# Optimization experiments

Hardware: AMD Instinct MI355X
Metric: run time of the kernel (lower is better)

The kernel has to match this reference:

```python
import jax, jax.numpy as jnp
import numpy as np

T, N, D, V = 512, 256, 1024, 128000  # total tokens, sampled tokens, d_model, vocab


def setup_inputs() -> dict:
    key = jax.random.key(0)
    k1, k2, k3, k4, k5 = jax.random.split(key, 5)
    hidden_states = jax.random.normal(k1, (T, D), dtype=jnp.float32)
    embedding = jax.random.normal(k2, (V, D), dtype=jnp.float32) * 0.02
    # temperatures in [0.5, 1.5): realistic, avoids divide blow-up (0.0 maps to 1.0 in source)
    temperatures = 0.5 + jax.random.uniform(k3, (N,), dtype=jnp.float32)
    # top_p in [0.5, 1.0)
    top_ps = 0.5 + 0.5 * jax.random.uniform(k4, (N,), dtype=jnp.float32)
    last_token_indices = jnp.sort(jax.random.randint(k5, (N,), 0, T))
    return {
        "hidden_states": hidden_states,
        "embedding": embedding,
        "temperatures": temperatures,
        "top_ps": top_ps,
        "last_token_indices": last_token_indices,
    }


def reference(hidden_states, embedding, temperatures, top_ps, last_token_indices):
    # gather last-token hidden states, project to vocab logits
    h = hidden_states[last_token_indices]              # [N, D]
    logits = jnp.einsum("nd,vd->nv", h, embedding)     # [N, V]
    # temperature softmax
    probs = jax.nn.softmax(logits / temperatures[:, None], axis=-1)
    # top-p: descending sort, cumsum, mask tail, renormalize, un-sort
    order = jnp.argsort(-probs, axis=-1)               # descending order indices
    probs_sort = jnp.take_along_axis(probs, order, axis=-1)
    cum = jnp.cumsum(probs_sort, axis=-1)
    mask = (cum - probs_sort) > top_ps[:, None]
    probs_sort = jnp.where(mask, 0.0, probs_sort)
    probs_sort = probs_sort / jnp.sum(probs_sort, axis=-1, keepdims=True)
    inv = jnp.argsort(order, axis=-1)                  # inverse permutation
    probs_f = jnp.take_along_axis(probs_sort, inv, axis=-1)
    # multinomial sampling (one token per row), fixed key for determinism
    tokens = jax.random.categorical(jax.random.key(42), jnp.log(probs_f + 1e-20), axis=-1)
    return probs_f, tokens
```

## Files before the change

### kernel.cpp

```cpp
#include <hip/hip_runtime.h>
#include <stdint.h>

#define N_TOK 256
#define D_MODEL 1024
#define VOCAB 128000
#define NV_ELEMS (256LL * 128000LL)
#define LIST_CAP 24576
#define GLIST_CAP 16384

typedef unsigned long long u64;
typedef uint32_t u32;
typedef __attribute__((ext_vector_type(8))) short bfrag;
typedef __attribute__((ext_vector_type(4))) float facc;

__device__ __forceinline__ uint32_t bf16_rne_bits(float x) {
    uint32_t u = __float_as_uint(x);
    return (u + 0x7fffu + ((u >> 16) & 1u)) >> 16;
}

__device__ __forceinline__ uint32_t rotl32(uint32_t x, int d) {
    return (x << d) | (x >> (32 - d));
}

__device__ __forceinline__ u32 mono32(u32 b) {
    return (b & 0x80000000u) ? ~b : (b | 0x80000000u);
}
__device__ __forceinline__ float unmono32(u32 k) {
    u32 b = (k & 0x80000000u) ? (k & 0x7FFFFFFFu) : ~k;
    return __uint_as_float(b);
}

__device__ __forceinline__ u64 fixmass(float rv) {
    return (u64)(rv * 1073741824.0f);
}

__device__ __forceinline__ uint2 tf_0_42(uint32_t c0, uint32_t c1) {
    const uint32_t ks0 = 0u, ks1 = 42u, ks2 = 0x1BD11BDAu ^ 42u;
    uint32_t x0 = c0 + ks0, x1 = c1 + ks1;
#define R4(a,b,c,d) \
    x0 += x1; x1 = rotl32(x1,a); x1 ^= x0; \
    x0 += x1; x1 = rotl32(x1,b); x1 ^= x0; \
    x0 += x1; x1 = rotl32(x1,c); x1 ^= x0; \
    x0 += x1; x1 = rotl32(x1,d); x1 ^= x0;
    R4(13,15,26,6)   x0 += ks1; x1 += ks2 + 1u;
    R4(17,29,16,24)  x0 += ks2; x1 += ks0 + 2u;
    R4(13,15,26,6)   x0 += ks0; x1 += ks1 + 3u;
    R4(17,29,16,24)  x0 += ks1; x1 += ks2 + 4u;
    R4(13,15,26,6)   x0 += ks2; x1 += ks0 + 5u;
#undef R4
    return make_uint2(x0, x1);
}

__device__ __forceinline__ uint32_t jax_bits(uint32_t j) {
    uint2 r = tf_0_42(0u, j);
    return r.x ^ r.y;
}

__device__ __forceinline__ float jax_gumbel(uint32_t bits) {
    const float TINY = 1.17549435e-38f;
    float u = __uint_as_float((bits >> 9) | 0x3f800000u) - 1.0f;
    u = u + TINY;
    u = fmaxf(TINY, u);
    return -__logf(-__logf(u));
}

__device__ __forceinline__ float rv_of(float l, float rinv) {
    return __expf(l * rinv);
}

__device__ __forceinline__ void async_copy16(const void* g, void* lbase, int lane) {
#if defined(__has_builtin) && __has_builtin(__builtin_amdgcn_global_load_lds)
    __builtin_amdgcn_global_load_lds((const uint32_t*)g, (uint32_t*)lbase, 16, 0, 0);
#else
    *(bfrag*)((char*)lbase + lane * 16) = *(const bfrag*)g;
#endif
}

__device__ __forceinline__ void scan_desc_u64(const u64* h, int nb, u64 carry, u64 P,
                                              int* outCb, u64* outSa) {
    int lane = (int)threadIdx.x & 63;
    int chunk = nb >> 6;
    int top = nb - 1 - lane * chunk;
    u64 ls = 0ull;
    for (int j = 0; j < chunk; ++j) ls += h[top - j];
    u64 incl = ls;
    for (int o = 1; o < 64; o <<= 1) {
        u64 v = __shfl_up(incl, o, 64);
        if (lane >= o) incl += v;
    }
    u64 s0 = carry + incl - ls;
    unsigned long long mask = __ballot(s0 + ls > P);
    if (mask == 0ull) {
        if (lane == 0) { *outCb = 0; *outSa = carry; }
    } else {
        int cstar = (int)__builtin_ctzll(mask);
        if (lane == cstar) {
            u64 sa = s0; int cb = 0;
            for (int j = 0; j < chunk; ++j) {
                int b = top - j;
                if (sa + h[b] > P) { cb = b; break; }
                sa += h[b];
            }
            *outCb = cb; *outSa = sa;
        }
    }
}

__global__ __launch_bounds__(256) void prep_a(
        const float* __restrict__ hidden, const int* __restrict__ idx,
        ushort* __restrict__ wsA) {
    const int m = blockIdx.x;
    const int t = threadIdx.x;
    const float* src = hidden + (long long)idx[m] * D_MODEL;
    const uint32_t swz = (uint32_t)((m & 7) << 4);
    for (int j = 0; j < 4; ++j) {
        int k = t * 4 + j;
        float x = src[k];
        uint32_t hb = bf16_rne_bits(x);
        float hf = __uint_as_float(hb << 16);
        uint32_t lb = bf16_rne_bits(x - hf);
        int kt = k >> 5, kk = k & 31, g = kk >> 3, e = kk & 7;
        char* img = (char*)wsA + (size_t)kt * 32768;
        uint32_t base = (uint32_t)(m * 128 + g * 32);
        *(ushort*)(img + ((base + 0) ^ swz) + e * 2) = (ushort)hb;
        *(ushort*)(img + ((base + 16) ^ swz) + e * 2) = (ushort)lb;
    }
}

__global__ __launch_bounds__(512) void gemm_mfma(
        const ushort* __restrict__ wsA, const float* __restrict__ emb,
        float* __restrict__ logits) {
    __shared__ __align__(16) ushort Aimg[16384];
    __shared__ __align__(16) ushort Bimg[16384];
    const int tid = (int)threadIdx.x;
    const int w = tid >> 6, l = tid & 63;
    const int wm = w >> 2, wn = w & 3;
    const int lr = l & 15, lg = l >> 4;
    const int v0 = blockIdx.x * 256;
    char* Ab = (char*)Aimg;
    char* Bb = (char*)Bimg;

    facc acc[8][4] = {};

    for (int kt = 0; kt < 32; ++kt) {
        __syncthreads();
        const char* asrc = (const char*)wsA + (size_t)kt * 32768;
#pragma unroll
        for (int i = 0; i < 4; ++i) {
            int off = w * 4096 + i * 1024;
            async_copy16(asrc + off + l * 16, Ab + off, l);
        }
        {
            int rb = tid >> 1, hf = tid & 1;
            const float* bs = emb + (size_t)(v0 + rb) * D_MODEL + kt * 32 + hf * 16;
            float4 q0 = *(const float4*)bs;
            float4 q1 = *(const float4*)(bs + 4);
            float4 q2 = *(const float4*)(bs + 8);
            float4 q3 = *(const float4*)(bs + 12);
            float xs[16] = {q0.x,q0.y,q0.z,q0.w, q1.x,q1.y,q1.z,q1.w,
                            q2.x,q2.y,q2.z,q2.w, q3.x,q3.y,q3.z,q3.w};
            uint32_t swz = (uint32_t)((rb & 7) << 4);
#pragma unroll
            for (int gg = 0; gg < 2; ++gg) {
                bfrag h, lo;
#pragma unroll
                for (int e = 0; e < 8; ++e) {
                    float x = xs[gg * 8 + e];
                    uint32_t hb = bf16_rne_bits(x);
                    float hfv = __uint_as_float(hb << 16);
                    uint32_t lb = bf16_rne_bits(x - hfv);
                    h[e] = (short)hb; lo[e] = (short)lb;
                }
                uint32_t base = (uint32_t)(rb * 128 + (hf * 2 + gg) * 32);
                *(bfrag*)(Bb + ((base + 0) ^ swz)) = h;
                *(bfrag*)(Bb + ((base + 16) ^ swz)) = lo;
            }
        }
        __syncthreads();
        bfrag bh[4], bl[4];
#pragma unroll
        for (int nj = 0; nj < 4; ++nj) {
            int rbf = wn * 64 + nj * 16 + lr;
            uint32_t swz = (uint32_t)((rbf & 7) << 4);
            uint32_t base = (uint32_t)(rbf * 128 + lg * 32);
            bh[nj] = *(const bfrag*)(Bb + ((base + 0) ^ swz));
            bl[nj] = *(const bfrag*)(Bb + ((base + 16) ^ swz));
        }
#pragma unroll
        for (int mi = 0; mi < 8; ++mi) {
            int r = wm * 128 + mi * 16 + lr;
            uint32_t swz = (uint32_t)((r & 7) << 4);
            uint32_t base = (uint32_t)(r * 128 + lg * 32);
            bfrag ah = *(const bfrag*)(Ab + ((base + 0) ^ swz));
            bfrag al = *(const bfrag*)(Ab + ((base + 16) ^ swz));
#pragma unroll
            for (int nj = 0; nj < 4; ++nj) {
                acc[mi][nj] = __builtin_amdgcn_mfma_f32_16x16x32_bf16(ah, bh[nj], acc[mi][nj], 0, 0, 0);
                acc[mi][nj] = __builtin_amdgcn_mfma_f32_16x16x32_bf16(ah, bl[nj], acc[mi][nj], 0, 0, 0);
                acc[mi][nj] = __builtin_amdgcn_mfma_f32_16x16x32_bf16(al, bh[nj], acc[mi][nj], 0, 0, 0);
            }
        }
    }
#pragma unroll
    for (int mi = 0; mi < 8; ++mi) {
        int mbase = wm * 128 + mi * 16 + lg * 4;
#pragma unroll
        for (int nj = 0; nj < 4; ++nj) {
            int v = v0 + wn * 64 + nj * 16 + lr;
#pragma unroll
            for (int reg = 0; reg < 4; ++reg)
                logits[(size_t)(mbase + reg) * VOCAB + v] = acc[mi][nj][reg];
        }
    }
}

__global__ __launch_bounds__(256) void gemm_kernel(
        const float* __restrict__ hidden, const int* __restrict__ idx,
        const float* __restrict__ emb, float* __restrict__ logits) {
    __shared__ float As[16][64];
    __shared__ float Bs[16][64];
    const int n0 = blockIdx.x * 64, v0 = blockIdx.y * 64;
    const int tid = threadIdx.x;
    const int tx = tid & 15, ty = tid >> 4;
    const int lr = tid >> 2, lk = (tid & 3) * 4;
    float acc[4][4] = {};
    const long long aRow = (long long)idx[n0 + lr] * D_MODEL + lk;
    const long long bRow = (long long)(v0 + lr) * D_MODEL + lk;
    for (int k0 = 0; k0 < D_MODEL; k0 += 16) {
        float4 av = *(const float4*)(hidden + aRow + k0);
        float4 bv = *(const float4*)(emb + bRow + k0);
        __syncthreads();
        As[lk + 0][lr] = av.x; As[lk + 1][lr] = av.y; As[lk + 2][lr] = av.z; As[lk + 3][lr] = av.w;
        Bs[lk + 0][lr] = bv.x; Bs[lk + 1][lr] = bv.y; Bs[lk + 2][lr] = bv.z; Bs[lk + 3][lr] = bv.w;
        __syncthreads();
#pragma unroll
        for (int kk = 0; kk < 16; ++kk) {
            float4 a = *(const float4*)&As[kk][ty * 4];
            float4 b = *(const float4*)&Bs[kk][tx * 4];
            float aa[4] = {a.x, a.y, a.z, a.w};
            float bb[4] = {b.x, b.y, b.z, b.w};
#pragma unroll
            for (int i = 0; i < 4; ++i)
#pragma unroll
                for (int j = 0; j < 4; ++j)
                    acc[i][j] += aa[i] * bb[j];
        }
    }
#pragma unroll
    for (int i = 0; i < 4; ++i) {
        float4 o = make_float4(acc[i][0], acc[i][1], acc[i][2], acc[i][3]);
        *(float4*)(logits + (long long)(n0 + ty * 4 + i) * VOCAB + (v0 + tx * 4)) = o;
    }
}

__global__ __launch_bounds__(512) void hist1_kernel(
        const float* __restrict__ probs, const float* __restrict__ temps,
        u64* __restrict__ ghist) {
    const int row = blockIdx.y, hb = blockIdx.x, tid = (int)threadIdx.x;
    __shared__ u64 h[4096];
    for (int i = tid; i < 4096; i += 512) h[i] = 0ull;
    __syncthreads();
    const float rinv = 1.0f / temps[row];
    const float4* R4 = (const float4*)(probs + (size_t)row * VOCAB);
    const int base4 = hb * 8000;
    for (int i = 0; i < 16; ++i) {
        int j = tid + i * 512;
        if (j < 8000) {
            float4 x = R4[base4 + j];
            float xs[4] = {x.x, x.y, x.z, x.w};
#pragma unroll
            for (int c = 0; c < 4; ++c) {
                u32 key = mono32(__float_as_uint(xs[c]));
                atomicAdd(&h[key >> 20], fixmass(rv_of(xs[c], rinv)));
            }
        }
    }
    __syncthreads();
    u64* gh = ghist + (size_t)row * 4096;
    for (int i = tid; i < 4096; i += 512)
        if (h[i]) atomicAdd(&gh[i], h[i]);
}

__global__ __launch_bounds__(64) void scan1_kernel(
        const u64* __restrict__ ghist, const float* __restrict__ topps,
        u64* __restrict__ rsP, u64* __restrict__ rsCarry, u32* __restrict__ rsCb) {
    const int row = blockIdx.x, lane = (int)threadIdx.x;
    const u64* h = ghist + (size_t)row * 4096;
    u64 S = 0ull;
    for (int j = lane; j < 4096; j += 64) S += h[j];
    for (int o = 32; o >= 1; o >>= 1) S += __shfl_xor(S, o, 64);
    const u64 P = (u64)((double)topps[row] * (double)S);
    __shared__ int sCb; __shared__ u64 sSa;
    scan_desc_u64(h, 4096, 0ull, P, &sCb, &sSa);
    __syncthreads();
    if (lane == 0) { rsP[row] = P; rsCarry[row] = sSa; rsCb[row] = (u32)sCb; }
}

__global__ __launch_bounds__(512) void compact_kernel(
        const float* __restrict__ probs, const u32* __restrict__ rsCb,
        u64* __restrict__ list, u32* __restrict__ listCnt) {
    const int row = blockIdx.y, hb = blockIdx.x, tid = (int)threadIdx.x;
    __shared__ u64 buf[4096];
    __shared__ u32 lcnt, gbase;
    const u32 cb1 = rsCb[row];
    const float4* R4 = (const float4*)(probs + (size_t)row * VOCAB);
    u64* lst = list + (size_t)row * GLIST_CAP;
    const int base4 = hb * 8000;
    if (tid == 0) lcnt = 0u;
    __syncthreads();
    for (int pair = 0; pair < 8; ++pair) {
#pragma unroll
        for (int s = 0; s < 2; ++s) {
            int j = tid + (pair * 2 + s) * 512;
            if (j < 8000) {
                float4 x = R4[base4 + j];
                float xs[4] = {x.x, x.y, x.z, x.w};
#pragma unroll
                for (int c = 0; c < 4; ++c) {
                    u32 key = mono32(__float_as_uint(xs[c]));
                    if ((key >> 20) == cb1) {
                        u32 pos = atomicAdd(&lcnt, 1u);
                        buf[pos] = ((u64)key << 32) | (u32)((base4 + j) * 4 + c);
                    }
                }
            }
        }
        __syncthreads();
        u32 n = lcnt;
        if (n) {
            if (tid == 0) gbase = atomicAdd(&listCnt[row], n);
            __syncthreads();
            u32 gb = gbase;
            for (u32 i2 = tid; i2 < n; i2 += 512) {
                u32 gpos = gb + i2;
                if (gpos < GLIST_CAP) lst[gpos] = buf[i2];
            }
        }
        __syncthreads();
        if (tid == 0) lcnt = 0u;
        __syncthreads();
    }
}

__global__ __launch_bounds__(1024) void resolve_kernel(
        const u64* __restrict__ list, const u32* __restrict__ listCnt,
        const u64* __restrict__ rsP, const u64* __restrict__ rsCarry,
        const u32* __restrict__ rsCb, const float* __restrict__ temps,
        u32* __restrict__ scTs, u32* __restrict__ scTieN,
        float* __restrict__ scInvSp, u32* __restrict__ tieKept) {
    const int row = blockIdx.x, tid = (int)threadIdx.x;
    __shared__ u64 h2[1024];
    __shared__ u32 c3[1024];
    __shared__ int sCb; __shared__ u64 sSa;
    __shared__ u32 sTc;
    __shared__ u32 tlist[1024];
    const u32 cnt = min(listCnt[row], (u32)GLIST_CAP);
    const u64 P = rsP[row];
    const float rinv = 1.0f / temps[row];
    const u64* lst = list + (size_t)row * GLIST_CAP;

    h2[tid] = 0ull;
    __syncthreads();
    for (u32 j = tid; j < cnt; j += 1024) {
        u32 key = (u32)(lst[j] >> 32);
        atomicAdd(&h2[(key >> 10) & 1023u], fixmass(rv_of(unmono32(key), rinv)));
    }
    __syncthreads();
    if (tid < 64) scan_desc_u64(h2, 1024, rsCarry[row], P, &sCb, &sSa);
    __syncthreads();
    const u32 cb2 = (u32)sCb; const u64 carry2 = sSa;
    __syncthreads();

    h2[tid] = 0ull; c3[tid] = 0u;
    __syncthreads();
    for (u32 j = tid; j < cnt; j += 1024) {
        u32 key = (u32)(lst[j] >> 32);
        if (((key >> 10) & 1023u) == cb2) {
            atomicAdd(&h2[key & 1023u], fixmass(rv_of(unmono32(key), rinv)));
            atomicAdd(&c3[key & 1023u], 1u);
        }
    }
    __syncthreads();
    if (tid < 64) scan_desc_u64(h2, 1024, carry2, P, &sCb, &sSa);
    __syncthreads();
    const int cb3 = sCb; const u64 sa3 = sSa;
    const u32 ts = (rsCb[row] << 20) | (cb2 << 10) | (u32)cb3;
    u32 cntb = c3[cb3]; if (cntb == 0u) cntb = 1u;
    const u64 tfq = fixmass(rv_of(unmono32(ts), rinv));
    const u64 rem = P - sa3;
    u32 mt;
    if (tfq == 0ull) mt = cntb;
    else {
        u64 q = rem / tfq;
        mt = (q >= (u64)(cntb - 1)) ? cntb : ((u32)q + 1u);
    }
    const u64 Spq = sa3 + (u64)mt * tfq;

    if (tid == 0) sTc = 0u;
    __syncthreads();
    for (u32 j = tid; j < cnt; j += 1024) {
        if ((u32)(lst[j] >> 32) == ts) {
            u32 pos = atomicAdd(&sTc, 1u);
            if (pos < 1024u) tlist[pos] = (u32)lst[j];
        }
    }
    __syncthreads();
    const u32 tn = min(sTc, 1024u);
    if ((u32)tid < tn) {
        u32 my = tlist[tid];
        u32 rank = 0;
        for (u32 j2 = 0; j2 < tn; ++j2) rank += (tlist[j2] < my) ? 1u : 0u;
        if (rank < mt) tieKept[(size_t)row * 1024 + rank] = my;
    }
    if (tid == 0) {
        scTs[row] = ts;
        scTieN[row] = min(mt, tn);
        scInvSp[row] = (float)(1073741824.0 / (double)Spq);
    }
}

__global__ __launch_bounds__(512) void final2_kernel(
        float* __restrict__ probs, const float* __restrict__ temps,
        const u32* __restrict__ scTs, const u32* __restrict__ scTieN,
        const float* __restrict__ scInvSp, const u32* __restrict__ tieKept,
        u64* __restrict__ argmax) {
    const int row = blockIdx.y, hb = blockIdx.x, tid = (int)threadIdx.x;
    __shared__ u32 tl[1024];
    __shared__ u64 wbest[8];
    const u32 ts = scTs[row], tieN = scTieN[row];
    const float invSp = scInvSp[row];
    const float rinv = 1.0f / temps[row];
    for (u32 i = tid; i < tieN; i += 512) tl[i] = tieKept[(size_t)row * 1024 + i];
    __syncthreads();
    float4* R4 = (float4*)(probs + (size_t)row * VOCAB);
    const u32 rowBase = (u32)row * (u32)VOCAB;
    const int base4 = hb * 8000;
    u64 best = 0ull;
    for (int i = 0; i < 16; ++i) {
        int j = tid + i * 512;
        if (j < 8000) {
            float4 x = R4[base4 + j];
            float xs[4] = {x.x, x.y, x.z, x.w};
            float4 out;
            float* op = (float*)&out;
#pragma unroll
            for (int c = 0; c < 4; ++c) {
                u32 key = mono32(__float_as_uint(xs[c]));
                u32 v = (u32)((base4 + j) * 4 + c);
                bool kept = key > ts;
                if (key == ts) {
                    kept = false;
                    for (u32 q2 = 0; q2 < tieN; ++q2)
                        if (tl[q2] == v) { kept = true; break; }
                }
                if (kept) {
                    float pf = rv_of(xs[c], rinv) * invSp;
                    op[c] = pf;
                    float g = jax_gumbel(jax_bits(rowBase + v));
                    float val = __logf(pf + 1e-20f) + g;
                    u64 pk = ((u64)mono32(__float_as_uint(val)) << 32) | (u32)(~v);
                    if (pk > best) best = pk;
                } else {
                    op[c] = 0.0f;
                }
            }
            R4[base4 + j] = out;
        }
    }
    for (int o = 32; o >= 1; o >>= 1) {
        u64 ob = __shfl_xor(best, o, 64);
        if (ob > best) best = ob;
    }
    if ((tid & 63) == 0) wbest[tid >> 6] = best;
    __syncthreads();
    if (tid == 0) {
        u64 b = wbest[0];
        for (int w2 = 1; w2 < 8; ++w2) if (wbest[w2] > b) b = wbest[w2];
        atomicMax(&argmax[row], b);
    }
}

__global__ void token_kernel(const u64* __restrict__ argmax, float* __restrict__ outTok) {
    int n = (int)threadIdx.x;
    if (n < N_TOK) outTok[n] = (float)(~(u32)argmax[n]);
}

__device__ __forceinline__ void scan_desc_wave(const float* h, int nb, float carry,
                                               float P, int* outCb, float* outSa) {
    int lane = (int)threadIdx.x & 63;
    int chunk = nb >> 6;
    int top = nb - 1 - lane * chunk;
    float ls = 0.0f;
    for (int j = 0; j < chunk; ++j) ls += h[top - j];
    float incl = ls;
    for (int o = 1; o < 64; o <<= 1) {
        float v = __shfl_up(incl, o, 64);
        if (lane >= o) incl += v;
    }
    float s0 = carry + incl - ls;
    unsigned long long mask = __ballot(s0 + ls > P);
    if (mask == 0ull) {
        if (lane == 63) { *outCb = 0; *outSa = carry + incl - h[0]; }
    } else {
        int cstar = (int)__builtin_ctzll(mask);
        if (lane == cstar) {
            float sa = s0; int cb = 0;
            for (int j = 0; j < chunk; ++j) {
                int b = top - j;
                if (sa + h[b] > P) { cb = b; break; }
                sa += h[b];
            }
            *outCb = cb; *outSa = sa;
        }
    }
}

__global__ __launch_bounds__(1024) void sample_kernel(
        float* __restrict__ probs, const float* __restrict__ temps,
        const float* __restrict__ topps, float* __restrict__ outTok) {
    const int row = blockIdx.x;
    const int tid = (int)threadIdx.x;
    float* L = probs + (long long)row * VOCAB;
    const float4* L4 = (const float4*)L;
    float4* L4w = (float4*)L;

    __shared__ float waveH[16][2048];
    __shared__ float hsum[2048];
    __shared__ uint32_t hcnt[1024];
    __shared__ float wred[16];
    __shared__ float aVal[16];
    __shared__ int aIdx[16];
    __shared__ uint32_t tieList[256];
    __shared__ int sCb;
    __shared__ float sSa;
    __shared__ float sP, sCarry1, sCarry2, sSp, sInvSp;
    __shared__ uint32_t sPref1, sCb2, sTsKey, sMt, sTieN, sCnt;
    uint32_t* keys = (uint32_t*)&waveH[4][0];

    const float t = temps[row];
    const float p = topps[row];
    const float rinv = 1.0f / t;

    for (int i = tid; i < 16 * 2048; i += 1024) ((float*)waveH)[i] = 0.0f;
    __syncthreads();
    {
        float* myH = waveH[tid >> 6];
#pragma unroll 2
        for (int i = 0; i < 31; ++i) {
            float4 x = L4[tid + i * 1024];
            float r0 = rv_of(x.x, rinv), r1 = rv_of(x.y, rinv);
            float r2 = rv_of(x.z, rinv), r3 = rv_of(x.w, rinv);
            atomicAdd(&myH[__float_as_uint(r0) >> 20], r0);
            atomicAdd(&myH[__float_as_uint(r1) >> 20], r1);
            atomicAdd(&myH[__float_as_uint(r2) >> 20], r2);
            atomicAdd(&myH[__float_as_uint(r3) >> 20], r3);
        }
        if (tid < 256) {
            float4 x = L4[31744 + tid];
            float r0 = rv_of(x.x, rinv), r1 = rv_of(x.y, rinv);
            float r2 = rv_of(x.z, rinv), r3 = rv_of(x.w, rinv);
            atomicAdd(&myH[__float_as_uint(r0) >> 20], r0);
            atomicAdd(&myH[__float_as_uint(r1) >> 20], r1);
            atomicAdd(&myH[__float_as_uint(r2) >> 20], r2);
            atomicAdd(&myH[__float_as_uint(r3) >> 20], r3);
        }
    }
    __syncthreads();
    {
        float a0 = 0.0f, a1 = 0.0f;
#pragma unroll
        for (int w2 = 0; w2 < 16; ++w2) { a0 += waveH[w2][tid]; a1 += waveH[w2][tid + 1024]; }
        hsum[tid] = a0; hsum[tid + 1024] = a1;
        float s = a0 + a1;
        for (int o = 32; o >= 1; o >>= 1) s += __shfl_xor(s, o, 64);
        if ((tid & 63) == 0) wred[tid >> 6] = s;
    }
    __syncthreads();
    if (tid == 0) {
        float tot = 0.0f;
        for (int w2 = 0; w2 < 16; ++w2) tot += wred[w2];
        sP = p * tot;
    }
    __syncthreads();
    if (tid < 64) scan_desc_wave(hsum, 2048, 0.0f, sP, &sCb, &sSa);
    __syncthreads();
    if (tid == 0) { sPref1 = (uint32_t)sCb; sCarry1 = sSa; sCnt = 0u; }
    __syncthreads();

    const uint32_t pref1 = sPref1;
    const float P = sP;
#pragma unroll 2
    for (int i = 0; i < 31; ++i) {
        float4 x = L4[tid + i * 1024];
        float rr[4] = {rv_of(x.x, rinv), rv_of(x.y, rinv), rv_of(x.z, rinv), rv_of(x.w, rinv)};
#pragma unroll
        for (int c = 0; c < 4; ++c) {
            uint32_t key = __float_as_uint(rr[c]);
            if ((key >> 20) == pref1) {
                uint32_t pos = atomicAdd(&sCnt, 1u);
                if (pos < LIST_CAP) keys[pos] = key;
            }
        }
    }
    if (tid < 256) {
        float4 x = L4[31744 + tid];
        float rr[4] = {rv_of(x.x, rinv), rv_of(x.y, rinv), rv_of(x.z, rinv), rv_of(x.w, rinv)};
#pragma unroll
        for (int c = 0; c < 4; ++c) {
            uint32_t key = __float_as_uint(rr[c]);
            if ((key >> 20) == pref1) {
                uint32_t pos = atomicAdd(&sCnt, 1u);
                if (pos < LIST_CAP) keys[pos] = key;
            }
        }
    }
    __syncthreads();
    const uint32_t K = sCnt;
    const bool inLds = (K <= LIST_CAP);

    if (tid < 1024) hsum[tid] = 0.0f;
    __syncthreads();
    if (inLds) {
        for (uint32_t j = tid; j < K; j += 1024) {
            uint32_t key = keys[j];
            atomicAdd(&hsum[(key >> 10) & 1023u], __uint_as_float(key));
        }
    } else {
        for (int i = 0; i < 125; ++i) {
            int v = tid + i * 1024;
            float rv = rv_of(L[v], rinv);
            uint32_t key = __float_as_uint(rv);
            if ((key >> 20) == pref1) atomicAdd(&hsum[(key >> 10) & 1023u], rv);
        }
    }
    __syncthreads();
    if (tid < 64) scan_desc_wave(hsum, 1024, sCarry1, P, &sCb, &sSa);
    __syncthreads();
    if (tid == 0) { sCb2 = (uint32_t)sCb; sCarry2 = sSa; }
    __syncthreads();

    const uint32_t cb2 = sCb2;
    if (tid < 1024) { hsum[tid] = 0.0f; hcnt[tid] = 0u; }
    __syncthreads();
    if (inLds) {
        for (uint32_t j = tid; j < K; j += 1024) {
            uint32_t key = keys[j];
            if (((key >> 10) & 1023u) == cb2) {
                atomicAdd(&hsum[key & 1023u], __uint_as_float(key));
                atomicAdd(&hcnt[key & 1023u], 1u);
            }
        }
    } else {
        const uint32_t pref2full = (pref1 << 10) | cb2;
        for (int i = 0; i < 125; ++i) {
            int v = tid + i * 1024;
            float rv = rv_of(L[v], rinv);
            uint32_t key = __float_as_uint(rv);
            if ((key >> 10) == pref2full) {
                atomicAdd(&hsum[key & 1023u], rv);
                atomicAdd(&hcnt[key & 1023u], 1u);
            }
        }
    }
    __syncthreads();
    if (tid < 64) scan_desc_wave(hsum, 1024, sCarry2, P, &sCb, &sSa);
    __syncthreads();
    if (tid == 0) {
        int cb3 = sCb; float sa3 = sSa;
        uint32_t ts = (pref1 << 20) | (cb2 << 10) | (uint32_t)cb3;
        uint32_t cnt = hcnt[cb3]; if (cnt == 0u) cnt = 1u;
        float tf = __uint_as_float(ts);
        uint32_t mt;
        float rem = P - sa3; if (rem < 0.0f) rem = 0.0f;
        if (!(tf > 0.0f)) mt = cnt;
        else {
            float q = floorf(rem / tf);
            mt = (q >= (float)(cnt - 1)) ? cnt : ((uint32_t)q + 1u);
        }
        sTsKey = ts; sMt = mt;
        sSp = sa3 + (float)mt * tf;
        sInvSp = 1.0f / sSp;
        sTieN = 0u;
    }
    __syncthreads();

    const uint32_t ts = sTsKey, mt = sMt;
    const float invSp = sInvSp;
    float bestV = -INFINITY;
    int bestI = 0x7FFFFFFF;
    const uint32_t rowBase = (uint32_t)row * (uint32_t)VOCAB;
    for (int i = 0; i < 32; ++i) {
        int f4i = (i < 31) ? (tid + i * 1024) : (31744 + tid);
        if (i == 31 && tid >= 256) break;
        float4 x = L4[f4i];
        float rr[4] = {rv_of(x.x, rinv), rv_of(x.y, rinv), rv_of(x.z, rinv), rv_of(x.w, rinv)};
        float4 out;
        float* op = (float*)&out;
#pragma unroll
        for (int c = 0; c < 4; ++c) {
            uint32_t key = __float_as_uint(rr[c]);
            int v = f4i * 4 + c;
            if (key > ts) {
                float pf = rr[c] * invSp;
                op[c] = pf;
                float g = jax_gumbel(jax_bits(rowBase + (uint32_t)v));
                float val = __logf(pf + 1e-20f) + g;
                if (val > bestV || (val == bestV && v < bestI)) { bestV = val; bestI = v; }
            } else if (key == ts) {
                op[c] = 0.0f;
                uint32_t pos = atomicAdd(&sTieN, 1u);
                if (pos < 256u) tieList[pos] = (uint32_t)v;
            } else {
                op[c] = 0.0f;
            }
        }
        L4w[f4i] = out;
    }
    __syncthreads();
    {
        const uint32_t tn = min(sTieN, 256u);
        if ((uint32_t)tid < tn) {
            uint32_t v = tieList[tid];
            uint32_t rank = 0;
            for (uint32_t j = 0; j < tn; ++j) rank += (tieList[j] < v) ? 1u : 0u;
            if (rank < mt) {
                float pf = __uint_as_float(ts) * invSp;
                L[v] = pf;
                float g = jax_gumbel(jax_bits(rowBase + v));
                float val = __logf(pf + 1e-20f) + g;
                if (val > bestV || (val == bestV && (int)v < bestI)) { bestV = val; bestI = (int)v; }
            }
        }
    }
    for (int o = 32; o >= 1; o >>= 1) {
        float ov = __shfl_xor(bestV, o, 64);
        int oi = __shfl_xor(bestI, o, 64);
        if (ov > bestV || (ov == bestV && oi < bestI)) { bestV = ov; bestI = oi; }
    }
    if ((tid & 63) == 0) { aVal[tid >> 6] = bestV; aIdx[tid >> 6] = bestI; }
    __syncthreads();
    if (tid == 0) {
        float bv = aVal[0]; int bi = aIdx[0];
        for (int w2 = 1; w2 < 16; ++w2) {
            if (aVal[w2] > bv || (aVal[w2] == bv && aIdx[w2] < bi)) { bv = aVal[w2]; bi = aIdx[w2]; }
        }
        outTok[row] = (float)bi;
    }
}

extern "C" void kernel_launch(void* const* d_in, const int* in_sizes, int n_in,
                              void* d_out, int out_size, void* d_ws, size_t ws_size,
                              hipStream_t stream) {
    const float* hidden = (const float*)d_in[0];
    const float* emb    = (const float*)d_in[1];
    const float* temps  = (const float*)d_in[2];
    const float* topps  = (const float*)d_in[3];
    const int*   idx    = (const int*)d_in[4];

    float* probs  = (float*)d_out;
    float* outTok = probs + NV_ELEMS;

    char* ws = (char*)d_ws;
    const bool wsGemm = ws_size >= (size_t)(1u << 20);
    const bool wsBig  = ws_size >= (size_t)(44u << 20);

    if (wsGemm) {
        ushort* wsA = (ushort*)ws;
        prep_a<<<N_TOK, 256, 0, stream>>>(hidden, idx, wsA);
        gemm_mfma<<<VOCAB / 256, 512, 0, stream>>>(wsA, emb, probs);
    } else {
        gemm_kernel<<<dim3(4, 2000), 256, 0, stream>>>(hidden, idx, emb, probs);
    }

    if (wsBig) {
        u64* ghist     = (u64*)(ws + (1u << 20));
        u64* list      = (u64*)(ws + (9u << 20));
        char* m        = ws + (41u << 20);
        u32* listCnt   = (u32*)(m);
        u32* rsCb      = (u32*)(m + 1024);
        u64* rsP       = (u64*)(m + 2048);
        u64* rsCarry   = (u64*)(m + 4096);
        u32* scTs      = (u32*)(m + 6144);
        u32* scTieN    = (u32*)(m + 7168);
        float* scInvSp = (float*)(m + 8192);
        u64* argmax    = (u64*)(m + 9216);
        u32* tieKept   = (u32*)(m + 16384);

        hipMemsetAsync(ghist, 0, (size_t)256 * 4096 * 8, stream);
        hipMemsetAsync(listCnt, 0, 1024, stream);
        hipMemsetAsync(argmax, 0, 2048, stream);

        hist1_kernel<<<dim3(4, N_TOK), 512, 0, stream>>>(probs, temps, ghist);
        scan1_kernel<<<N_TOK, 64, 0, stream>>>(ghist, topps, rsP, rsCarry, rsCb);
        compact_kernel<<<dim3(4, N_TOK), 512, 0, stream>>>(probs, rsCb, list, listCnt);
        resolve_kernel<<<N_TOK, 1024, 0, stream>>>(list, listCnt, rsP, rsCarry, rsCb,
                                                   temps, scTs, scTieN, scInvSp, tieKept);
        final2_kernel<<<dim3(4, N_TOK), 512, 0, stream>>>(probs, temps, scTs, scTieN,
                                                          scInvSp, tieKept, argmax);
        token_kernel<<<1, 256, 0, stream>>>(argmax, outTok);
    } else {
        sample_kernel<<<N_TOK, 1024, 0, stream>>>(probs, temps, topps, outTok);
    }
}
```

Measured before the change: 460.2 us.

## Shrink MFMA GEMM tile to 256x64, prefetch B registers, hoist memsets

The bf16x3 MFMA GEMM now uses 256-thread blocks that each cover 64 vocab columns instead of 512-thread blocks covering 256. This launches 2000 blocks instead of 500 and targets 4 blocks per CU for better occupancy and load balance. Each thread prefetches the next K-step's embedding floats into registers to overlap global loads with compute. The workspace memsets move ahead of the GEMM launch. The cost is that each block reloads the full A tile for only 64 columns, so LDS traffic per FLOP goes up.

```diff
diff --git a/kernel.cpp b/kernel.cpp
--- a/kernel.cpp
+++ b/kernel.cpp
@@ -127,68 +127,66 @@
     }
 }
 
-__global__ __launch_bounds__(512) void gemm_mfma(
+__global__ __launch_bounds__(256, 4) void gemm_mfma(
         const ushort* __restrict__ wsA, const float* __restrict__ emb,
         float* __restrict__ logits) {
     __shared__ __align__(16) ushort Aimg[16384];
-    __shared__ __align__(16) ushort Bimg[16384];
+    __shared__ __align__(16) ushort Bimg[8192];
     const int tid = (int)threadIdx.x;
     const int w = tid >> 6, l = tid & 63;
-    const int wm = w >> 2, wn = w & 3;
     const int lr = l & 15, lg = l >> 4;
-    const int v0 = blockIdx.x * 256;
+    const int v0 = blockIdx.x * 64;
     char* Ab = (char*)Aimg;
     char* Bb = (char*)Bimg;
 
-    facc acc[8][4] = {};
+    facc acc[4][4] = {};
+
+    const int rb = tid >> 2, g = tid & 3;
+    const float* bbase = emb + (size_t)(v0 + rb) * D_MODEL + g * 8;
+    float4 q0 = *(const float4*)(bbase);
+    float4 q1 = *(const float4*)(bbase + 4);
 
     for (int kt = 0; kt < 32; ++kt) {
         __syncthreads();
         const char* asrc = (const char*)wsA + (size_t)kt * 32768;
 #pragma unroll
-        for (int i = 0; i < 4; ++i) {
-            int off = w * 4096 + i * 1024;
+        for (int i = 0; i < 8; ++i) {
+            int off = w * 8192 + i * 1024;
             async_copy16(asrc + off + l * 16, Ab + off, l);
         }
+        float4 n0 = q0, n1 = q1;
+        if (kt < 31) {
+            n0 = *(const float4*)(bbase + (kt + 1) * 32);
+            n1 = *(const float4*)(bbase + (kt + 1) * 32 + 4);
+        }
         {
-            int rb = tid >> 1, hf = tid & 1;
-            const float* bs = emb + (size_t)(v0 + rb) * D_MODEL + kt * 32 + hf * 16;
-            float4 q0 = *(const float4*)bs;
-            float4 q1 = *(const float4*)(bs + 4);
-            float4 q2 = *(const float4*)(bs + 8);
-            float4 q3 = *(const float4*)(bs + 12);
-            float xs[16] = {q0.x,q0.y,q0.z,q0.w, q1.x,q1.y,q1.z,q1.w,
-                            q2.x,q2.y,q2.z,q2.w, q3.x,q3.y,q3.z,q3.w};
+            float xs[8] = {q0.x, q0.y, q0.z, q0.w, q1.x, q1.y, q1.z, q1.w};
+            bfrag h, lo;
+#pragma unroll
+            for (int e = 0; e < 8; ++e) {
+                uint32_t hb = bf16_rne_bits(xs[e]);
+                float hf = __uint_as_float(hb << 16);
+                uint32_t lb = bf16_rne_bits(xs[e] - hf);
+                h[e] = (short)hb; lo[e] = (short)lb;
+            }
             uint32_t swz = (uint32_t)((rb & 7) << 4);
-#pragma unroll
-            for (int gg = 0; gg < 2; ++gg) {
-                bfrag h, lo;
-#pragma unroll
-                for (int e = 0; e < 8; ++e) {
-                    float x = xs[gg * 8 + e];
-                    uint32_t hb = bf16_rne_bits(x);
-                    float hfv = __uint_as_float(hb << 16);
-                    uint32_t lb = bf16_rne_bits(x - hfv);
-                    h[e] = (short)hb; lo[e] = (short)lb;
-                }
-                uint32_t base = (uint32_t)(rb * 128 + (hf * 2 + gg) * 32);
-                *(bfrag*)(Bb + ((base + 0) ^ swz)) = h;
-                *(bfrag*)(Bb + ((base + 16) ^ swz)) = lo;
-            }
+            uint32_t base = (uint32_t)(rb * 128 + g * 32);
+            *(bfrag*)(Bb + ((base + 0) ^ swz)) = h;
+            *(bfrag*)(Bb + ((base + 16) ^ swz)) = lo;
         }
         __syncthreads();
         bfrag bh[4], bl[4];
 #pragma unroll
         for (int nj = 0; nj < 4; ++nj) {
-            int rbf = wn * 64 + nj * 16 + lr;
+            int rbf = nj * 16 + lr;
             uint32_t swz = (uint32_t)((rbf & 7) << 4);
             uint32_t base = (uint32_t)(rbf * 128 + lg * 32);
             bh[nj] = *(const bfrag*)(Bb + ((base + 0) ^ swz));
             bl[nj] = *(const bfrag*)(Bb + ((base + 16) ^ swz));
         }
 #pragma unroll
-        for (int mi = 0; mi < 8; ++mi) {
-            int r = wm * 128 + mi * 16 + lr;
+        for (int mi = 0; mi < 4; ++mi) {
+            int r = w * 64 + mi * 16 + lr;
             uint32_t swz = (uint32_t)((r & 7) << 4);
             uint32_t base = (uint32_t)(r * 128 + lg * 32);
             bfrag ah = *(const bfrag*)(Ab + ((base + 0) ^ swz));
@@ -200,13 +198,14 @@
                 acc[mi][nj] = __builtin_amdgcn_mfma_f32_16x16x32_bf16(al, bh[nj], acc[mi][nj], 0, 0, 0);
             }
         }
-    }
-#pragma unroll
-    for (int mi = 0; mi < 8; ++mi) {
-        int mbase = wm * 128 + mi * 16 + lg * 4;
+        q0 = n0; q1 = n1;
+    }
+#pragma unroll
+    for (int mi = 0; mi < 4; ++mi) {
+        int mbase = w * 64 + mi * 16 + lg * 4;
 #pragma unroll
         for (int nj = 0; nj < 4; ++nj) {
-            int v = v0 + wn * 64 + nj * 16 + lr;
+            int v = v0 + nj * 16 + lr;
 #pragma unroll
             for (int reg = 0; reg < 4; ++reg)
                 logits[(size_t)(mbase + reg) * VOCAB + v] = acc[mi][nj][reg];
@@ -764,10 +763,18 @@
     const bool wsGemm = ws_size >= (size_t)(1u << 20);
     const bool wsBig  = ws_size >= (size_t)(44u << 20);
 
+    if (wsBig) {
+        u64* ghist   = (u64*)(ws + (1u << 20));
+        char* m      = ws + (41u << 20);
+        hipMemsetAsync(ghist, 0, (size_t)256 * 4096 * 8, stream);
+        hipMemsetAsync(m, 0, 1024, stream);
+        hipMemsetAsync(m + 9216, 0, 2048, stream);
+    }
+
     if (wsGemm) {
         ushort* wsA = (ushort*)ws;
         prep_a<<<N_TOK, 256, 0, stream>>>(hidden, idx, wsA);
-        gemm_mfma<<<VOCAB / 256, 512, 0, stream>>>(wsA, emb, probs);
+        gemm_mfma<<<VOCAB / 64, 256, 0, stream>>>(wsA, emb, probs);
     } else {
         gemm_kernel<<<dim3(4, 2000), 256, 0, stream>>>(hidden, idx, emb, probs);
     }
@@ -786,10 +793,6 @@
         u64* argmax    = (u64*)(m + 9216);
         u32* tieKept   = (u32*)(m + 16384);
 
-        hipMemsetAsync(ghist, 0, (size_t)256 * 4096 * 8, stream);
-        hipMemsetAsync(listCnt, 0, 1024, stream);
-        hipMemsetAsync(argmax, 0, 2048, stream);
-
         hist1_kernel<<<dim3(4, N_TOK), 512, 0, stream>>>(probs, temps, ghist);
         scan1_kernel<<<N_TOK, 64, 0, stream>>>(ghist, topps, rsP, rsCarry, rsCb);
         compact_kernel<<<dim3(4, N_TOK), 512, 0, stream>>>(probs, rsCb, list, listCnt);
```

Result: slower. 499.7 us (+8.6%).
